# Kernel tuning notes

Measured on AMD Instinct MI355X. Metric: run time of the kernel, lower is better.

## Reference

```python
import jax, jax.numpy as jnp
import numpy as np

T, B, D, H = 1024, 8, 1024, 16
NH = D // H  # 64, per-head width (nhid)
W_SCALE = 0.02


def setup_inputs() -> dict:
    key = jax.random.key(0)
    ks = jax.random.split(key, 10)
    return {
        "input_tensor": jax.random.normal(ks[0], (T, B, D), jnp.float32),
        "keys_vector": jax.random.normal(ks[1], (T, B, D), jnp.float32),
        "values_vector": jax.random.normal(ks[2], (T, B, D), jnp.float32),
        # per-head projection weights: [H, D, NH]
        "Wq": jax.random.normal(ks[3], (H, D, NH), jnp.float32) * W_SCALE,
        "bq": jnp.zeros((H, NH), jnp.float32),
        "Wk": jax.random.normal(ks[4], (H, D, NH), jnp.float32) * W_SCALE,
        "bk": jnp.zeros((H, NH), jnp.float32),
        "Wv": jax.random.normal(ks[5], (H, D, NH), jnp.float32) * W_SCALE,
        "bv": jnp.zeros((H, NH), jnp.float32),
        # output projection after concatenating heads
        "Wo": jax.random.normal(ks[6], (D, D), jnp.float32) * W_SCALE,
        "bo": jnp.zeros((D,), jnp.float32),
        "mask": 1,  # True: causal (growing key slice per timestep)
    }


def reference(input_tensor, keys_vector, values_vector, Wq, bq, Wk, bk, Wv, bv, Wo, bo, mask):
    # Vectorized equivalent of the per-timestep loop: query at step t attends
    # to keys/values[:t+1] when mask is set, else to the full sequence.
    q = jnp.einsum('tbd,hdk->tbhk', input_tensor, Wq) + bq   # [T,B,H,NH]
    k = jnp.einsum('sbd,hdk->sbhk', keys_vector, Wk) + bk    # [T,B,H,NH]
    v = jnp.einsum('sbd,hdk->sbhk', values_vector, Wv) + bv  # [T,B,H,NH]

    scale = 1.0 / jnp.sqrt(jnp.float32(NH))
    scores = jnp.einsum('tbhk,sbhk->bhts', q, k) * scale     # [B,H,T,T]
    if mask:
        causal = jnp.tril(jnp.ones((T, T), dtype=bool))      # s <= t
        scores = jnp.where(causal[None, None], scores, jnp.float32(-1e9))
    attn = jax.nn.softmax(scores, axis=-1)                   # over key dim s

    out = jnp.einsum('bhts,sbhk->tbhk', attn, v)             # [T,B,H,NH]
    out = out.reshape(T, B, D)                               # concat heads
    return out @ Wo.T + bo                                   # [T,B,D]
```

## Files before the change

kernel.cpp:

```cpp
#include <hip/hip_runtime.h>

typedef short bf16x8 __attribute__((ext_vector_type(8)));
typedef float f32x4 __attribute__((ext_vector_type(4)));
typedef float f32x16 __attribute__((ext_vector_type(16)));

typedef const __attribute__((address_space(1))) void* gptr_t;
typedef __attribute__((address_space(3))) void* sptr_t;

#define Z16 {0.f,0.f,0.f,0.f,0.f,0.f,0.f,0.f,0.f,0.f,0.f,0.f,0.f,0.f,0.f,0.f}
#define VMCNT(n) asm volatile("s_waitcnt vmcnt(" #n ")" ::: "memory")
#define LGKM0 asm volatile("s_waitcnt lgkmcnt(0)" ::: "memory")
#define SCHEDB __builtin_amdgcn_sched_barrier(0)
#define SBAR __builtin_amdgcn_s_barrier()

__device__ __forceinline__ void glds16(const void* g, void* s) {
  __builtin_amdgcn_global_load_lds((gptr_t)g, (sptr_t)s, 16, 0, 0);
}

__device__ __forceinline__ unsigned short f2bf(float x) {
  unsigned u = __float_as_uint(x);
  u = u + 0x7fffu + ((u >> 16) & 1u);
  return (unsigned short)(u >> 16);
}

__device__ __forceinline__ unsigned packbf(float lo, float hi) {
  return (unsigned)f2bf(lo) | (((unsigned)f2bf(hi)) << 16);
}

__global__ void cvtall(const float* __restrict__ X, const float* __restrict__ KY,
                       const float* __restrict__ VY, const float* __restrict__ Wo,
                       unsigned short* __restrict__ XB, unsigned short* __restrict__ WOB) {
  int stride = gridDim.x * blockDim.x;
  for (int i = blockIdx.x * blockDim.x + threadIdx.x; i < 6553600; i += stride) {
    const float* in; unsigned short* out; int k;
    if (i < 2097152)      { in = X;  out = XB;            k = i; }
    else if (i < 4194304) { in = KY; out = XB + 8388608;  k = i - 2097152; }
    else if (i < 6291456) { in = VY; out = XB + 16777216; k = i - 4194304; }
    else                  { in = Wo; out = WOB;           k = i - 6291456; }
    float4 v = ((const float4*)in)[k];
    uint2 r;
    r.x = packbf(v.x, v.y);
    r.y = packbf(v.z, v.w);
    ((uint2*)out)[k] = r;
  }
}

__global__ __launch_bounds__(256) void wtrans(const float* __restrict__ Wq,
                                              const float* __restrict__ Wk,
                                              const float* __restrict__ Wv,
                                              unsigned short* __restrict__ WT) {
  int m = blockIdx.y >> 4, h = blockIdx.y & 15, d0 = blockIdx.x * 64;
  const float* src = (m == 0 ? Wq : (m == 1 ? Wk : Wv)) + (size_t)h * 65536;
  __shared__ float tile[64][65];
  int c = (threadIdx.x & 15) * 4, r0 = threadIdx.x >> 4;
#pragma unroll
  for (int rr = 0; rr < 4; ++rr) {
    int dr = rr * 16 + r0;
    float4 v = *(const float4*)(src + (size_t)(d0 + dr) * 64 + c);
    tile[dr][c + 0] = v.x; tile[dr][c + 1] = v.y;
    tile[dr][c + 2] = v.z; tile[dr][c + 3] = v.w;
  }
  __syncthreads();
#pragma unroll
  for (int rr = 0; rr < 4; ++rr) {
    int kr = rr * 16 + r0;
    uint2 pk;
    pk.x = packbf(tile[c + 0][kr], tile[c + 1][kr]);
    pk.y = packbf(tile[c + 2][kr], tile[c + 3][kr]);
    *(uint2*)(WT + ((size_t)(m * 1024 + h * 64 + kr)) * 1024 + d0 + c) = pk;
  }
}

__global__ __launch_bounds__(256) void gemm_qkv(const unsigned short* __restrict__ Ab,
                                                const unsigned short* __restrict__ Bb,
                                                const float* __restrict__ bi0,
                                                const float* __restrict__ bi1,
                                                const float* __restrict__ bi2,
                                                unsigned short* __restrict__ outp) {
  const int K = 1024;
  int z = blockIdx.z;
  const unsigned short* A = Ab + (size_t)z * 8192 * 1024;
  const unsigned short* BT = Bb + (size_t)z * 1024 * 1024;
  const float* bias = z == 0 ? bi0 : (z == 1 ? bi1 : bi2);
  int m0 = blockIdx.x * 128, n0 = blockIdx.y * 128;
  __shared__ __align__(16) char lds[65536];
  int tid = threadIdx.x, w = tid >> 6, l = tid & 63, ml = l & 15, hi = l >> 4;
  int wr = (w >> 1) * 64, wc = (w & 1) * 64;
  int srow = l >> 3;
  int kphys = (l & 7) << 4;
  f32x4 acc[4][4] = {};
#pragma unroll
  for (int i = 0; i < 4; ++i) {
    int c = w * 4 + i;
    int row = c * 8 + srow;
    int klog = kphys ^ ((row & 7) << 4);
    glds16((const char*)(A + (size_t)(m0 + row) * K) + klog, lds + c * 1024);
    glds16((const char*)(BT + (size_t)(n0 + row) * K) + klog, lds + 16384 + c * 1024);
  }
  __syncthreads();
  int cur = 0;
  for (int kt16 = 0; kt16 < 16; ++kt16) {
    if (kt16 + 1 < 16) {
      char* nb = lds + (cur ^ 1) * 32768;
      int kt = (kt16 + 1) * 64;
#pragma unroll
      for (int i = 0; i < 4; ++i) {
        int c = w * 4 + i;
        int row = c * 8 + srow;
        int klog = kphys ^ ((row & 7) << 4);
        glds16((const char*)(A + (size_t)(m0 + row) * K + kt) + klog, nb + c * 1024);
        glds16((const char*)(BT + (size_t)(n0 + row) * K + kt) + klog, nb + 16384 + c * 1024);
      }
    }
    char* As = lds + cur * 32768;
    char* Bs = As + 16384;
#pragma unroll
    for (int ks = 0; ks < 2; ++ks) {
      bf16x8 af[4], bfr[4];
#pragma unroll
      for (int mi = 0; mi < 4; ++mi) {
        int row = wr + mi * 16 + ml;
        af[mi] = *(const bf16x8*)(As + row * 128 + ((ks * 64 + (hi << 4)) ^ ((row & 7) << 4)));
      }
#pragma unroll
      for (int ni = 0; ni < 4; ++ni) {
        int row = wc + ni * 16 + ml;
        bfr[ni] = *(const bf16x8*)(Bs + row * 128 + ((ks * 64 + (hi << 4)) ^ ((row & 7) << 4)));
      }
      __builtin_amdgcn_s_setprio(1);
#pragma unroll
      for (int mi = 0; mi < 4; ++mi)
#pragma unroll
        for (int ni = 0; ni < 4; ++ni)
          acc[mi][ni] = __builtin_amdgcn_mfma_f32_16x16x32_bf16(af[mi], bfr[ni], acc[mi][ni], 0, 0, 0);
      __builtin_amdgcn_s_setprio(0);
    }
    __syncthreads();
    cur ^= 1;
  }
#pragma unroll
  for (int mi = 0; mi < 4; ++mi) {
#pragma unroll
    for (int ni = 0; ni < 4; ++ni) {
      int col = wc + ni * 16 + ml;
      float bv = bias[n0 + col];
#pragma unroll
      for (int r = 0; r < 4; ++r) {
        int row = wr + mi * 16 + (hi << 2) + r;
        float v = acc[mi][ni][r] + bv;
        float pv = __shfl_xor(v, 1);
        unsigned pk = (ml & 1) ? packbf(pv, v) : packbf(v, pv);
        *(unsigned*)(lds + row * 256 + (((col * 2) & ~3) ^ ((row & 7) << 4))) = pk;
      }
    }
  }
  __syncthreads();
  unsigned short* ob = outp + (size_t)z * 8388608;
  if (z != 2) {
    int rr = tid >> 1, hh = tid & 1;
    int t = (m0 + rr) >> 3, b = (m0 + rr) & 7;
    int hg = (n0 >> 6) + hh;
    unsigned short* dst = ob + (size_t)(b * 16 + hg) * 65536 + (size_t)t * 64;
#pragma unroll
    for (int j = 0; j < 8; ++j) {
      uint4 d = *(uint4*)(lds + rr * 256 + ((hh * 128 + j * 16) ^ ((rr & 7) << 4)));
      *(uint4*)(dst + j * 8) = d;
    }
  } else {
    int t0 = m0 >> 3;
#pragma unroll
    for (int q = 0; q < 4; ++q) {
      int run = q * 256 + tid;
      int k = run & 63;
      int bh2 = run >> 6;
      int b = bh2 >> 1, hh = bh2 & 1;
      int colb = (hh * 64 + k) * 2;
      union { unsigned short u[16]; uint4 v[2]; } tmp;
#pragma unroll
      for (int tp = 0; tp < 16; ++tp) {
        int rowt = tp * 8 + b;
        tmp.u[tp] = *(unsigned short*)(lds + rowt * 256 + (colb ^ ((b & 7) << 4)));
      }
      int hg = (n0 >> 6) + hh;
      unsigned short* dst = ob + (size_t)(b * 16 + hg) * 65536 + (size_t)k * 1024 + t0;
      *(uint4*)dst = tmp.v[0];
      *(uint4*)(dst + 8) = tmp.v[1];
    }
  }
}

__global__ __launch_bounds__(256) void gemm_out(const unsigned short* __restrict__ A,
                                                const unsigned short* __restrict__ BT,
                                                const float* __restrict__ bias,
                                                float* __restrict__ outp) {
  const int K = 1024;
  int m0 = blockIdx.x * 128, n0 = blockIdx.y * 128;
  __shared__ __align__(16) char lds[32768];
  char* As = lds;
  char* Bs = lds + 16384;
  int tid = threadIdx.x, w = tid >> 6, l = tid & 63, ml = l & 15, hi = l >> 4;
  int wr = (w >> 1) * 64, wc = (w & 1) * 64;
  int srow = l >> 3;
  int kphys = (l & 7) << 4;
  f32x4 acc[4][4] = {};
  for (int kt = 0; kt < K; kt += 64) {
    __syncthreads();
#pragma unroll
    for (int i = 0; i < 4; ++i) {
      int c = w * 4 + i;
      int row = c * 8 + srow;
      int klog = kphys ^ ((row & 7) << 4);
      glds16((const char*)(A + (size_t)(m0 + row) * K + kt) + klog, As + c * 1024);
      glds16((const char*)(BT + (size_t)(n0 + row) * K + kt) + klog, Bs + c * 1024);
    }
    __syncthreads();
#pragma unroll
    for (int ks = 0; ks < 2; ++ks) {
      bf16x8 af[4], bfr[4];
#pragma unroll
      for (int mi = 0; mi < 4; ++mi) {
        int row = wr + mi * 16 + ml;
        af[mi] = *(const bf16x8*)(As + row * 128 + ((ks * 64 + (hi << 4)) ^ ((row & 7) << 4)));
      }
#pragma unroll
      for (int ni = 0; ni < 4; ++ni) {
        int row = wc + ni * 16 + ml;
        bfr[ni] = *(const bf16x8*)(Bs + row * 128 + ((ks * 64 + (hi << 4)) ^ ((row & 7) << 4)));
      }
      __builtin_amdgcn_s_setprio(1);
#pragma unroll
      for (int mi = 0; mi < 4; ++mi)
#pragma unroll
        for (int ni = 0; ni < 4; ++ni)
          acc[mi][ni] = __builtin_amdgcn_mfma_f32_16x16x32_bf16(af[mi], bfr[ni], acc[mi][ni], 0, 0, 0);
      __builtin_amdgcn_s_setprio(0);
    }
  }
#pragma unroll
  for (int mi = 0; mi < 4; ++mi) {
#pragma unroll
    for (int ni = 0; ni < 4; ++ni) {
      int col = n0 + wc + ni * 16 + ml;
      float bv = bias[col];
#pragma unroll
      for (int r = 0; r < 4; ++r) {
        int row = m0 + wr + mi * 16 + (hi << 2) + r;
        outp[(size_t)row * 1024 + col] = acc[mi][ni][r] + bv;
      }
    }
  }
}

__global__ __launch_bounds__(512, 4) void attn_k(const unsigned short* __restrict__ Qp,
                                                 const unsigned short* __restrict__ Kp,
                                                 const unsigned short* __restrict__ VTp,
                                                 unsigned short* __restrict__ Op,
                                                 const int* __restrict__ maskp) {
  int lin = blockIdx.x;
  int xcd = lin & 7, idx = lin >> 3;
  int bh = xcd + 8 * (idx >> 2);
  int j = idx & 3;
  const size_t base = (size_t)bh * 65536;
  int tid = threadIdx.x, w = tid >> 6, l = tid & 63;
  int ml5 = l & 31, hi1 = l >> 5;
  int half = w & 1, pi = w >> 1;
  int stripe = (pi == 0) ? j : (pi == 1) ? (15 - j) : (pi == 2) ? (7 - j) : (8 + j);
  int tw0 = stripe * 64 + half * 32;
  int t_glob = tw0 + ml5;
  __shared__ __align__(16) char lds[32768];
  int msk = *maskp;
  const float CE = 0.18033688011112042f;
  bf16x8 bq[4];
#pragma unroll
  for (int kd = 0; kd < 4; ++kd)
    bq[kd] = *(const bf16x8*)(Qp + base + (size_t)t_glob * 64 + kd * 16 + hi1 * 8);
  f32x16 o0 = Z16, o1 = Z16;
  float m_run = -3e38f, l_run = 0.f;
  int nt = msk ? (16 - j) : 16;
  int diag = stripe;
  int srow = l >> 3, kphys = (l & 7) << 4;
  int row = w * 8 + srow;
  int klog = kphys ^ (srow << 4);
  int swz = (ml5 & 7) << 4;
  glds16((const char*)(Kp + base + (size_t)row * 64) + klog, lds + w * 1024);
  glds16((const char*)(VTp + base + (size_t)row * 1024) + klog, lds + 8192 + w * 1024);
  int cur = 0;
  for (int st = 0; st < nt; ++st) {
    if (st + 1 < nt) {
      char* nb = lds + (cur ^ 1) * 16384;
      glds16((const char*)(Kp + base + (size_t)((st + 1) * 64 + row) * 64) + klog, nb + w * 1024);
      glds16((const char*)(VTp + base + (size_t)row * 1024 + (st + 1) * 64) + klog, nb + 8192 + w * 1024);
      VMCNT(4);
    } else {
      VMCNT(0);
    }
    SCHEDB; SBAR; SCHEDB;
    if (!msk || st <= diag) {
      char* Ks = lds + cur * 16384;
      char* Vs = Ks + 8192;
      f32x16 s0 = Z16, s1 = Z16;
      __builtin_amdgcn_s_setprio(1);
#pragma unroll
      for (int kd = 0; kd < 4; ++kd) {
        int koff = kd * 32 + hi1 * 16;
        bf16x8 a0 = *(const bf16x8*)(Ks + ml5 * 128 + (koff ^ swz));
        bf16x8 a1 = *(const bf16x8*)(Ks + (32 + ml5) * 128 + (koff ^ swz));
        s0 = __builtin_amdgcn_mfma_f32_32x32x16_bf16(a0, bq[kd], s0, 0, 0, 0);
        s1 = __builtin_amdgcn_mfma_f32_32x32x16_bf16(a1, bq[kd], s1, 0, 0, 0);
      }
      __builtin_amdgcn_s_setprio(0);
      if (msk && st == diag) {
#pragma unroll
        for (int r = 0; r < 16; ++r) {
          int sl = st * 64 + (r & 3) + 8 * (r >> 2) + 4 * hi1;
          if (sl > t_glob) s0[r] = -1e30f;
          if (sl + 32 > t_glob) s1[r] = -1e30f;
        }
      }
      float t8[8];
#pragma unroll
      for (int r = 0; r < 8; ++r)
        t8[r] = fmaxf(fmaxf(s0[r], s0[r + 8]), fmaxf(s1[r], s1[r + 8]));
      float tm = fmaxf(fmaxf(fmaxf(t8[0], t8[1]), fmaxf(t8[2], t8[3])),
                       fmaxf(fmaxf(t8[4], t8[5]), fmaxf(t8[6], t8[7])));
      tm = fmaxf(tm, __shfl_xor(tm, 32));
      float m_old = m_run;
      float m_new = fmaxf(m_old, tm);
      m_run = m_new;
      float sc2 = exp2f((m_old - m_new) * CE);
      float mC = m_new * CE;
#pragma unroll
      for (int r = 0; r < 16; ++r) {
        s0[r] = exp2f(fmaf(s0[r], CE, -mC));
        s1[r] = exp2f(fmaf(s1[r], CE, -mC));
      }
      float a8[8];
#pragma unroll
      for (int r = 0; r < 8; ++r)
        a8[r] = (s0[r] + s0[r + 8]) + (s1[r] + s1[r + 8]);
      float ps = ((a8[0] + a8[1]) + (a8[2] + a8[3])) + ((a8[4] + a8[5]) + (a8[6] + a8[7]));
      ps += __shfl_xor(ps, 32);
      l_run = l_run * sc2 + ps;
#pragma unroll
      for (int r = 0; r < 16; ++r) { o0[r] *= sc2; o1[r] *= sc2; }
      unsigned cc0[4][2], cc1[4][2];
#pragma unroll
      for (int q = 0; q < 4; ++q) {
        cc0[q][0] = packbf(s0[4 * q + 0], s0[4 * q + 1]);
        cc0[q][1] = packbf(s0[4 * q + 2], s0[4 * q + 3]);
        cc1[q][0] = packbf(s1[4 * q + 0], s1[4 * q + 1]);
        cc1[q][1] = packbf(s1[4 * q + 2], s1[4 * q + 3]);
      }
#define CCa(a, p) ((a) < 4 ? cc0[(a) & 3][p] : cc1[(a) & 3][p])
      union U4 { unsigned u[4]; bf16x8 v; };
      bf16x8 pb[4];
#pragma unroll
      for (int kb = 0; kb < 4; ++kb) {
        U4 t;
#pragma unroll
        for (int p = 0; p < 2; ++p) {
          unsigned x = CCa(2 * kb, p), y = CCa(2 * kb + 1, p);
          unsigned v = hi1 ? x : y;
          unsigned wv = hi1 ? y : x;
          unsigned vs = __shfl_xor(v, 32);
          t.u[p]     = hi1 ? vs : wv;
          t.u[2 + p] = hi1 ? wv : vs;
        }
        pb[kb] = t.v;
      }
#undef CCa
      __builtin_amdgcn_s_setprio(1);
#pragma unroll
      for (int kb = 0; kb < 4; ++kb) {
        int koff = kb * 32 + hi1 * 16;
        bf16x8 v0 = *(const bf16x8*)(Vs + ml5 * 128 + (koff ^ swz));
        bf16x8 v1 = *(const bf16x8*)(Vs + (32 + ml5) * 128 + (koff ^ swz));
        o0 = __builtin_amdgcn_mfma_f32_32x32x16_bf16(v0, pb[kb], o0, 0, 0, 0);
        o1 = __builtin_amdgcn_mfma_f32_32x32x16_bf16(v1, pb[kb], o1, 0, 0, 0);
      }
      __builtin_amdgcn_s_setprio(0);
    }
    SCHEDB; LGKM0; SBAR;
    cur ^= 1;
  }
  float rl = 1.0f / l_run;
  int b = bh >> 4, h = bh & 15;
  unsigned short* orow = Op + (size_t)(t_glob * 8 + b) * 1024 + h * 64;
#pragma unroll
  for (int q2 = 0; q2 < 4; ++q2) {
    uint2 pk0, pk1;
    pk0.x = packbf(o0[4 * q2 + 0] * rl, o0[4 * q2 + 1] * rl);
    pk0.y = packbf(o0[4 * q2 + 2] * rl, o0[4 * q2 + 3] * rl);
    *(uint2*)(orow + 4 * hi1 + 8 * q2) = pk0;
    pk1.x = packbf(o1[4 * q2 + 0] * rl, o1[4 * q2 + 1] * rl);
    pk1.y = packbf(o1[4 * q2 + 2] * rl, o1[4 * q2 + 3] * rl);
    *(uint2*)(orow + 32 + 4 * hi1 + 8 * q2) = pk1;
  }
}

extern "C" void kernel_launch(void* const* d_in, const int* in_sizes, int n_in,
                              void* d_out, int out_size, void* d_ws, size_t ws_size,
                              hipStream_t stream) {
  const float* X  = (const float*)d_in[0];
  const float* KY = (const float*)d_in[1];
  const float* VY = (const float*)d_in[2];
  const float* Wq = (const float*)d_in[3];
  const float* bq = (const float*)d_in[4];
  const float* Wk = (const float*)d_in[5];
  const float* bk = (const float*)d_in[6];
  const float* Wv = (const float*)d_in[7];
  const float* bv = (const float*)d_in[8];
  const float* Wo = (const float*)d_in[9];
  const float* bo = (const float*)d_in[10];
  const int* mask = (const int*)d_in[11];
  char* ws = (char*)d_ws;
  unsigned short* XB  = (unsigned short*)(ws);
  unsigned short* WT  = (unsigned short*)(ws + 48ll * 1024 * 1024);
  unsigned short* WOB = (unsigned short*)(ws + 54ll * 1024 * 1024);
  unsigned short* QP  = (unsigned short*)(ws + 56ll * 1024 * 1024);
  unsigned short* OP  = (unsigned short*)(ws + 104ll * 1024 * 1024);

  cvtall<<<2048, 256, 0, stream>>>(X, KY, VY, Wo, XB, WOB);
  wtrans<<<dim3(16, 48), 256, 0, stream>>>(Wq, Wk, Wv, WT);
  gemm_qkv<<<dim3(64, 8, 3), 256, 0, stream>>>(XB, WT, bq, bk, bv, QP);
  attn_k<<<512, 512, 0, stream>>>(QP, QP + 8388608, QP + 16777216, OP, mask);
  gemm_out<<<dim3(64, 8, 1), 256, 0, stream>>>(OP, WOB, bo, (float*)d_out);
}
```

Baseline: 199.7 us.

## Double-buffer output GEMM, swizzle GEMM tile order, lazily rescale softmax

The output projection GEMM now uses a double-buffered LDS pipeline, prefetching the next K tile while computing the current one, like the QKV GEMM already does. Both GEMMs remap block indices to group M tiles for better L2 reuse. The attention kernel skips the running-max rescale of the output accumulators unless some lane's new max exceeds the old max by more than a threshold. This trades a larger LDS footprint and a bounded exponent growth for fewer stalls and less per-tile multiply work.

```diff
diff --git a/kernel.cpp b/kernel.cpp
--- a/kernel.cpp
+++ b/kernel.cpp
@@ -82,7 +82,10 @@
   const unsigned short* A = Ab + (size_t)z * 8192 * 1024;
   const unsigned short* BT = Bb + (size_t)z * 1024 * 1024;
   const float* bias = z == 0 ? bi0 : (z == 1 ? bi1 : bi2);
-  int m0 = blockIdx.x * 128, n0 = blockIdx.y * 128;
+  int lin = blockIdx.y * 64 + blockIdx.x;
+  int mt = (lin & 7) * 8 + ((lin >> 3) & 7);
+  int nt = lin >> 6;
+  int m0 = mt * 128, n0 = nt * 128;
   __shared__ __align__(16) char lds[65536];
   int tid = threadIdx.x, w = tid >> 6, l = tid & 63, ml = l & 15, hi = l >> 4;
   int wr = (w >> 1) * 64, wc = (w & 1) * 64;
@@ -194,26 +197,41 @@
                                                 const float* __restrict__ bias,
                                                 float* __restrict__ outp) {
   const int K = 1024;
-  int m0 = blockIdx.x * 128, n0 = blockIdx.y * 128;
-  __shared__ __align__(16) char lds[32768];
-  char* As = lds;
-  char* Bs = lds + 16384;
+  int lin = blockIdx.y * 64 + blockIdx.x;
+  int mt = (lin & 7) * 8 + ((lin >> 3) & 7);
+  int nt = lin >> 6;
+  int m0 = mt * 128, n0 = nt * 128;
+  __shared__ __align__(16) char lds[65536];
   int tid = threadIdx.x, w = tid >> 6, l = tid & 63, ml = l & 15, hi = l >> 4;
   int wr = (w >> 1) * 64, wc = (w & 1) * 64;
   int srow = l >> 3;
   int kphys = (l & 7) << 4;
   f32x4 acc[4][4] = {};
-  for (int kt = 0; kt < K; kt += 64) {
-    __syncthreads();
-#pragma unroll
-    for (int i = 0; i < 4; ++i) {
-      int c = w * 4 + i;
-      int row = c * 8 + srow;
-      int klog = kphys ^ ((row & 7) << 4);
-      glds16((const char*)(A + (size_t)(m0 + row) * K + kt) + klog, As + c * 1024);
-      glds16((const char*)(BT + (size_t)(n0 + row) * K + kt) + klog, Bs + c * 1024);
-    }
-    __syncthreads();
+#pragma unroll
+  for (int i = 0; i < 4; ++i) {
+    int c = w * 4 + i;
+    int row = c * 8 + srow;
+    int klog = kphys ^ ((row & 7) << 4);
+    glds16((const char*)(A + (size_t)(m0 + row) * K) + klog, lds + c * 1024);
+    glds16((const char*)(BT + (size_t)(n0 + row) * K) + klog, lds + 16384 + c * 1024);
+  }
+  __syncthreads();
+  int cur = 0;
+  for (int kt16 = 0; kt16 < 16; ++kt16) {
+    if (kt16 + 1 < 16) {
+      char* nb = lds + (cur ^ 1) * 32768;
+      int kt = (kt16 + 1) * 64;
+#pragma unroll
+      for (int i = 0; i < 4; ++i) {
+        int c = w * 4 + i;
+        int row = c * 8 + srow;
+        int klog = kphys ^ ((row & 7) << 4);
+        glds16((const char*)(A + (size_t)(m0 + row) * K + kt) + klog, nb + c * 1024);
+        glds16((const char*)(BT + (size_t)(n0 + row) * K + kt) + klog, nb + 16384 + c * 1024);
+      }
+    }
+    char* As = lds + cur * 32768;
+    char* Bs = As + 16384;
 #pragma unroll
     for (int ks = 0; ks < 2; ++ks) {
       bf16x8 af[4], bfr[4];
@@ -235,6 +253,8 @@
           acc[mi][ni] = __builtin_amdgcn_mfma_f32_16x16x32_bf16(af[mi], bfr[ni], acc[mi][ni], 0, 0, 0);
       __builtin_amdgcn_s_setprio(0);
     }
+    __syncthreads();
+    cur ^= 1;
   }
 #pragma unroll
   for (int mi = 0; mi < 4; ++mi) {
@@ -324,11 +344,15 @@
       float tm = fmaxf(fmaxf(fmaxf(t8[0], t8[1]), fmaxf(t8[2], t8[3])),
                        fmaxf(fmaxf(t8[4], t8[5]), fmaxf(t8[6], t8[7])));
       tm = fmaxf(tm, __shfl_xor(tm, 32));
-      float m_old = m_run;
-      float m_new = fmaxf(m_old, tm);
-      m_run = m_new;
-      float sc2 = exp2f((m_old - m_new) * CE);
-      float mC = m_new * CE;
+      if (!__all(tm <= m_run + 8.0f)) {
+        float m_new = fmaxf(m_run, tm);
+        float sc2 = exp2f((m_run - m_new) * CE);
+        l_run *= sc2;
+#pragma unroll
+        for (int r = 0; r < 16; ++r) { o0[r] *= sc2; o1[r] *= sc2; }
+        m_run = m_new;
+      }
+      float mC = m_run * CE;
 #pragma unroll
       for (int r = 0; r < 16; ++r) {
         s0[r] = exp2f(fmaf(s0[r], CE, -mC));
@@ -340,9 +364,7 @@
         a8[r] = (s0[r] + s0[r + 8]) + (s1[r] + s1[r + 8]);
       float ps = ((a8[0] + a8[1]) + (a8[2] + a8[3])) + ((a8[4] + a8[5]) + (a8[6] + a8[7]));
       ps += __shfl_xor(ps, 32);
-      l_run = l_run * sc2 + ps;
-#pragma unroll
-      for (int r = 0; r < 16; ++r) { o0[r] *= sc2; o1[r] *= sc2; }
+      l_run += ps;
       unsigned cc0[4][2], cc1[4][2];
 #pragma unroll
       for (int q = 0; q < 4; ++q) {
```

New measurement: 193.8 us. -2.9%, faster.
